# Optimization experiments

Measured on AMD Instinct MI355X. Metric: run time of the kernel, lower is better.

## Reference

```python
import jax, jax.numpy as jnp
import numpy as np

WS = 8
HEADS = 8


def _conv3(x, w, groups=1):
    return jax.lax.conv_general_dilated(
        x, w, (1, 1), 'SAME',
        dimension_numbers=('NCHW', 'OIHW', 'NCHW'),
        feature_group_count=groups)


def _bn(x, g, b, eps=1e-5):
    # training-mode batchnorm (batch statistics), per-channel over (B,H,W)
    m = x.mean(axis=(0, 2, 3), keepdims=True)
    v = x.var(axis=(0, 2, 3), keepdims=True)
    return (x - m) * jax.lax.rsqrt(v + eps) * g[None, :, None, None] + b[None, :, None, None]


def _relu6(x):
    return jnp.clip(x, 0.0, 6.0)


def _forward(x, w_iem, g_iem, b_iem, w_nem, g_nem, b_nem,
             w_iem_dw, w_nem_dw, w_q, w_k, w_v, w_proj, temperature):
    b, C, hp, wp = x.shape
    heads = temperature.shape[1]
    d = C // heads
    ws = WS
    nh, nw = hp // ws, wp // ws  # H,W chosen divisible by ws -> no padding

    iem_out = _relu6(_bn(_conv3(x, w_iem), g_iem, b_iem))
    illumination_map = _conv3(iem_out, w_iem_dw, groups=C)
    nem_out = _relu6(_bn(_conv3(x, w_nem), g_nem, b_nem))
    noise_map = _conv3(nem_out, w_nem_dw, groups=C)

    illum_scalar = illumination_map.mean(axis=1, keepdims=True)  # [b,1,H,W]
    noise_scalar = noise_map.mean(axis=1, keepdims=True)

    # 1x1 convs as channel matmuls
    q = jnp.einsum('oc,bchw->bohw', w_q, illumination_map)
    k = jnp.einsum('oc,bchw->bohw', w_k, noise_map)
    v = jnp.einsum('oc,bchw->bohw', w_v, x)

    def to_windows(t):  # [b,C,H,W] -> [b,heads,nh,nw,ws*ws,d]
        t = t.reshape(b, heads, d, hp, wp).transpose(0, 1, 3, 4, 2)
        t = t.reshape(b, heads, nh, ws, nw, ws, d).transpose(0, 1, 2, 4, 3, 5, 6)
        return t.reshape(b, heads, nh, nw, ws * ws, d)

    def scalar_to_windows(t):  # [b,1,H,W] -> [b,1,nh,nw,ws*ws,1]
        t = t.reshape(b, 1, nh, ws, nw, ws).transpose(0, 1, 2, 4, 3, 5)
        return t.reshape(b, 1, nh, nw, ws * ws, 1)

    qw, kw, vw = to_windows(q), to_windows(k), to_windows(v)
    illum_w = scalar_to_windows(illum_scalar)
    noise_w = scalar_to_windows(noise_scalar)

    qw = qw / jnp.maximum(jnp.linalg.norm(qw, axis=-1, keepdims=True), 1e-12)
    kw = kw / jnp.maximum(jnp.linalg.norm(kw, axis=-1, keepdims=True), 1e-12)
    qw = qw * (1.0 + illum_w)
    kw = kw * jnp.clip(1.0 - noise_w, 0.0, 1.0)

    scale = d ** (-0.5)
    attn = jnp.einsum('bhnmqd,bhnmkd->bhnmqk', qw, kw) * scale
    attn = attn * temperature  # temperature: [1,heads,1,1,1,1]
    attn = jax.nn.softmax(attn, axis=-1)
    outw = jnp.einsum('bhnmqk,bhnmkd->bhnmqd', attn, vw)

    outw = outw.reshape(b, heads, nh, nw, ws, ws, d).transpose(0, 1, 6, 2, 4, 3, 5)
    out = outw.reshape(b, C, hp, wp)
    return jnp.einsum('oc,bchw->bohw', w_proj, out)


def setup_inputs() -> dict:
    key = jax.random.key(0)
    ks = jax.random.split(key, 10)
    C = 256
    B, H, W = 2, 256, 256

    def w(k, shape):
        return jax.random.normal(k, shape, jnp.float32) * 0.05

    return {
        'x': jax.random.normal(ks[0], (B, C, H, W), jnp.float32),
        'w_iem': w(ks[1], (C, C, 3, 3)),
        'g_iem': jnp.ones((C,), jnp.float32),
        'b_iem': jnp.zeros((C,), jnp.float32),
        'w_nem': w(ks[2], (C, C, 3, 3)),
        'g_nem': jnp.ones((C,), jnp.float32),
        'b_nem': jnp.zeros((C,), jnp.float32),
        'w_iem_dw': w(ks[3], (C, 1, 3, 3)),
        'w_nem_dw': w(ks[4], (C, 1, 3, 3)),
        'w_q': w(ks[5], (C, C)),
        'w_k': w(ks[6], (C, C)),
        'w_v': w(ks[7], (C, C)),
        'w_proj': w(ks[8], (C, C)),
        'temperature': jnp.ones((1, HEADS, 1, 1, 1, 1), jnp.float32),
    }


def reference(x, w_iem, g_iem, b_iem, w_nem, g_nem, b_nem,
              w_iem_dw, w_nem_dw, w_q, w_k, w_v, w_proj, temperature):
    return _forward(x, w_iem, g_iem, b_iem, w_nem, g_nem, b_nem,
                    w_iem_dw, w_nem_dw, w_q, w_k, w_v, w_proj, temperature)
```

## Files before the change

### kernel.cpp

```cpp
#include <hip/hip_runtime.h>
#include <math.h>

constexpr int Bn  = 2;
constexpr int C   = 256;
constexpr int H   = 256;
constexpr int W   = 256;
constexpr int HW  = H * W;
constexpr size_t CHW = (size_t)C * HW;

typedef __bf16 bf16x8 __attribute__((ext_vector_type(8)));
typedef float  f32x4  __attribute__((ext_vector_type(4)));

__device__ __forceinline__ unsigned short f2bf(float f) {
    unsigned int u = __float_as_uint(f);
    u += 0x7fffu + ((u >> 16) & 1u);
    return (unsigned short)(u >> 16);
}
__device__ __forceinline__ float bf2f(unsigned short h) {
    return __uint_as_float(((unsigned int)h) << 16);
}
__device__ __forceinline__ float bflo(unsigned int u) { return __uint_as_float(u << 16); }
__device__ __forceinline__ float bfhi(unsigned int u) { return __uint_as_float(u & 0xffff0000u); }

__device__ __forceinline__ bf16x8 u2b(uint4 u) {
    union { uint4 a; bf16x8 b; } c; c.a = u; return c.b;
}

__device__ __forceinline__ void gld_lds16(const void* g, void* lds) {
    __builtin_amdgcn_global_load_lds(
        (const __attribute__((address_space(1))) unsigned int*)g,
        (__attribute__((address_space(3))) unsigned int*)lds, 16, 0, 0);
}

__device__ __forceinline__ int swz2048(int bid) {
    return ((bid & 7) << 8) | (bid >> 3);
}

__global__ __launch_bounds__(256) void packx_k(
    const float* __restrict__ x, unsigned short* __restrict__ xT)
{
    __shared__ float tl[64][65];
    const int id = blockIdx.x;
    const int ct = id & 3;
    const size_t px0 = (size_t)(id >> 2) * 64;
    const int b  = (int)(px0 >> 16);
    const int hw = (int)(px0 & 65535);
    const int c0 = ct * 64;
    const int t  = threadIdx.x;

    {
        const int cl = t >> 2, pseg = t & 3;
        const float* src = x + ((size_t)(b * C + c0 + cl)) * HW + hw + pseg * 16;
#pragma unroll
        for (int i = 0; i < 4; i++) {
            float4 v = *(const float4*)(src + i * 4);
            tl[cl][pseg * 16 + i * 4 + 0] = v.x;
            tl[cl][pseg * 16 + i * 4 + 1] = v.y;
            tl[cl][pseg * 16 + i * 4 + 2] = v.z;
            tl[cl][pseg * 16 + i * 4 + 3] = v.w;
        }
    }
    __syncthreads();
    {
        const int pl = t >> 2, csec = t & 3;
        __attribute__((aligned(16))) unsigned short rv[16];
#pragma unroll
        for (int j = 0; j < 16; j++) rv[j] = f2bf(tl[csec * 16 + j][pl]);
        unsigned short* dst = xT + (px0 + pl) * C + c0 + csec * 16;
        *(uint4*)dst       = *(const uint4*)&rv[0];
        *(uint4*)(dst + 8) = *(const uint4*)&rv[8];
    }
}

__global__ __launch_bounds__(256) void pack_k(
    const float* __restrict__ w, unsigned short* __restrict__ out, int taps)
{
    const int e = blockIdx.x * 256 + threadIdx.x;
    const int kslot = e & 31;
    const int ocl   = (e >> 5) & 127;
    const int icc   = (e >> 12) & 7;
    const int oct   = (e >> 15) & 1;
    const int off   = e >> 16;
    const int oc = oct * 128 + ocl;
    const int q  = kslot >> 3, j = kslot & 7;
    const int ic = icc * 32 + ((q ^ ((ocl >> 2) & 3)) << 3) + j;
    out[e] = f2bf(w[((size_t)oc * C + ic) * taps + off]);
}

__global__ __launch_bounds__(256, 2) void conv2_k(
    const unsigned short* __restrict__ xT,
    const unsigned short* __restrict__ Wp0, const unsigned short* __restrict__ Wp1,
    unsigned short* __restrict__ out0, unsigned short* __restrict__ out1,
    const unsigned short* __restrict__ zbuf)
{
    __shared__ unsigned short As[2][2][128 * 32];
    __shared__ unsigned short Bs[2][128 * 32];

    const int id  = swz2048(blockIdx.x);
    const int oct = id & 1;
    const int ch  = (id >> 1) & 1;
    const int r   = (id >> 2) & 255;
    const int b   = id >> 10;
    const int px0 = ch * 128;

    const int t  = threadIdx.x;
    const int wv = t >> 6;
    const int l  = t & 63;
    const int wm = (wv >> 1) * 64;
    const int wn = (wv & 1) * 64;

    const int qp = (l >> 4) ^ ((l >> 2) & 3);
    int a_off[4], b_off[4];
#pragma unroll
    for (int i = 0; i < 4; i++) {
        a_off[i] = (wm + i * 16 + (l & 15)) * 64 + qp * 16;
        b_off[i] = (wn + i * 16 + (l & 15)) * 64 + qp * 16;
    }
    const int spx_base = wv * 32 + (l >> 2);
    const int skk0 = (((l & 3) ^ (l >> 4)) << 3);

    const int off_lo = (r == 0) ? 3 : 0;
    const int off_hi = (r == 255) ? 6 : 9;

    f32x4 acc[2][4][4];
#pragma unroll
    for (int s = 0; s < 2; s++)
#pragma unroll
        for (int i = 0; i < 4; i++)
#pragma unroll
            for (int j = 0; j < 4; j++) acc[s][i][j] = (f32x4){0.f, 0.f, 0.f, 0.f};

#pragma unroll 1
    for (int off = off_lo; off < off_hi; ++off) {
        const int dy = off / 3, dx = off - dy * 3;
        const int rr = r + dy - 1;
        const size_t rowpix = (size_t)(b * HW) + (size_t)rr * W;
#pragma unroll 1
        for (int ip = 0; ip < 4; ++ip) {
            __syncthreads();
            const size_t wofs = ((size_t)(((off * 2 + oct) * 8 + ip * 2)) * 4096) * 2
                                + wv * 2048 + l * 16;
#pragma unroll
            for (int kc = 0; kc < 2; kc++) {
                char* A0 = (char*)As[0][kc] + wv * 2048;
                char* A1 = (char*)As[1][kc] + wv * 2048;
                const size_t o = wofs + (size_t)kc * 8192;
                gld_lds16((const char*)Wp0 + o, A0);
                gld_lds16((const char*)Wp0 + o + 1024, A0 + 1024);
                gld_lds16((const char*)Wp1 + o, A1);
                gld_lds16((const char*)Wp1 + o + 1024, A1 + 1024);
                const int ic0 = (ip * 2 + kc) * 32;
                char* BsB = (char*)Bs[kc] + wv * 2048;
#pragma unroll
                for (int i = 0; i < 2; i++) {
                    const int px = spx_base + i * 16;
                    const int cx = px0 + px + dx - 1;
                    const void* g = ((unsigned)cx > 255u)
                        ? (const void*)zbuf
                        : (const void*)(xT + ((rowpix + cx) * C + ic0 + skk0));
                    gld_lds16(g, BsB + i * 1024);
                }
            }
            asm volatile("s_waitcnt vmcnt(0)" ::: "memory");
            __syncthreads();
#pragma unroll
            for (int kc = 0; kc < 2; kc++) {
                bf16x8 af0[4], af1[4], bfr[4];
#pragma unroll
                for (int i = 0; i < 4; i++) {
                    af0[i] = *(const bf16x8*)((const char*)As[0][kc] + a_off[i]);
                    af1[i] = *(const bf16x8*)((const char*)As[1][kc] + a_off[i]);
                }
#pragma unroll
                for (int i = 0; i < 4; i++)
                    bfr[i] = *(const bf16x8*)((const char*)Bs[kc] + b_off[i]);
#pragma unroll
                for (int mi = 0; mi < 4; mi++)
#pragma unroll
                    for (int nj = 0; nj < 4; nj++) {
                        acc[0][mi][nj] = __builtin_amdgcn_mfma_f32_16x16x32_bf16(
                            af0[mi], bfr[nj], acc[0][mi][nj], 0, 0, 0);
                        acc[1][mi][nj] = __builtin_amdgcn_mfma_f32_16x16x32_bf16(
                            af1[mi], bfr[nj], acc[1][mi][nj], 0, 0, 0);
                    }
            }
        }
    }

    const int colpx = px0 + wn + (l & 15);
    const int rowoc = oct * 128 + wm + (l >> 4) * 4;
#pragma unroll
    for (int s = 0; s < 2; s++) {
        unsigned short* ob = s ? out1 : out0;
#pragma unroll
        for (int mi = 0; mi < 4; mi++) {
#pragma unroll
            for (int nj = 0; nj < 4; nj++) {
#pragma unroll
                for (int rg = 0; rg < 4; rg++) {
                    const int oc = rowoc + mi * 16 + rg;
                    const int px = colpx + nj * 16;
                    const size_t idx = ((size_t)(b * C + oc)) * HW + (size_t)r * W + px;
                    ob[idx] = f2bf(acc[s][mi][nj][rg]);
                }
            }
        }
    }
}

__global__ __launch_bounds__(256, 2) void gemm2_k(
    const unsigned short* __restrict__ qin, const unsigned short* __restrict__ kin,
    const unsigned short* __restrict__ Wpq, const unsigned short* __restrict__ Wpk,
    unsigned short* __restrict__ outq, unsigned short* __restrict__ outk)
{
    __shared__ unsigned short As[2][2][128 * 32];
    __shared__ unsigned short Bs[2][2][128 * 32];

    const int id  = swz2048(blockIdx.x);
    const int oct = id & 1;
    const int ch  = (id >> 1) & 1;
    const int r   = (id >> 2) & 255;
    const int b   = id >> 10;
    const int px0 = ch * 128;

    const int t  = threadIdx.x;
    const int wv = t >> 6;
    const int l  = t & 63;
    const int wm = (wv >> 1) * 64;
    const int wn = (wv & 1) * 64;

    const int qp = (l >> 4) ^ ((l >> 2) & 3);
    int a_off[4], b_off[4];
#pragma unroll
    for (int i = 0; i < 4; i++) {
        a_off[i] = (wm + i * 16 + (l & 15)) * 64 + qp * 16;
        b_off[i] = (wn + i * 16 + (l & 15)) * 64 + qp * 16;
    }
    const int spx_base = wv * 32 + (l >> 2);
    const int skk0 = (((l & 3) ^ (l >> 4)) << 3);

    const size_t rowpix = (size_t)(b * HW) + (size_t)r * W;

    f32x4 acc[2][4][4];
#pragma unroll
    for (int s = 0; s < 2; s++)
#pragma unroll
        for (int i = 0; i < 4; i++)
#pragma unroll
            for (int j = 0; j < 4; j++) acc[s][i][j] = (f32x4){0.f, 0.f, 0.f, 0.f};

#pragma unroll 1
    for (int ip = 0; ip < 4; ++ip) {
        __syncthreads();
#pragma unroll
        for (int kc = 0; kc < 2; kc++) {
            const int icc = ip * 2 + kc;
            const size_t wofs = ((size_t)(oct * 8 + icc) * 4096) * 2 + wv * 2048 + l * 16;
            char* Aq = (char*)As[0][kc] + wv * 2048;
            char* Ak = (char*)As[1][kc] + wv * 2048;
            gld_lds16((const char*)Wpq + wofs, Aq);
            gld_lds16((const char*)Wpq + wofs + 1024, Aq + 1024);
            gld_lds16((const char*)Wpk + wofs, Ak);
            gld_lds16((const char*)Wpk + wofs + 1024, Ak + 1024);
            const int ic0 = icc * 32;
            char* Bq = (char*)Bs[0][kc] + wv * 2048;
            char* Bk = (char*)Bs[1][kc] + wv * 2048;
#pragma unroll
            for (int i = 0; i < 2; i++) {
                const int cx = px0 + spx_base + i * 16;
                gld_lds16((const void*)(qin + ((rowpix + cx) * C + ic0 + skk0)), Bq + i * 1024);
                gld_lds16((const void*)(kin + ((rowpix + cx) * C + ic0 + skk0)), Bk + i * 1024);
            }
        }
        asm volatile("s_waitcnt vmcnt(0)" ::: "memory");
        __syncthreads();
#pragma unroll
        for (int kc = 0; kc < 2; kc++) {
#pragma unroll
            for (int s = 0; s < 2; s++) {
                bf16x8 af[4], bfr[4];
#pragma unroll
                for (int i = 0; i < 4; i++) {
                    af[i]  = *(const bf16x8*)((const char*)As[s][kc] + a_off[i]);
                    bfr[i] = *(const bf16x8*)((const char*)Bs[s][kc] + b_off[i]);
                }
#pragma unroll
                for (int mi = 0; mi < 4; mi++)
#pragma unroll
                    for (int nj = 0; nj < 4; nj++)
                        acc[s][mi][nj] = __builtin_amdgcn_mfma_f32_16x16x32_bf16(
                            af[mi], bfr[nj], acc[s][mi][nj], 0, 0, 0);
            }
        }
    }

    const int colpx = px0 + wn + (l & 15);
    const int rowoc = oct * 128 + wm + (l >> 4) * 4;
    const size_t pxg = (size_t)(b * HW) + (size_t)r * W;
#pragma unroll
    for (int s = 0; s < 2; s++) {
        unsigned short* ob = s ? outk : outq;
#pragma unroll
        for (int mi = 0; mi < 4; mi++) {
#pragma unroll
            for (int nj = 0; nj < 4; nj++) {
                __attribute__((aligned(8))) unsigned short rv[4];
#pragma unroll
                for (int rg = 0; rg < 4; rg++) rv[rg] = f2bf(acc[s][mi][nj][rg]);
                const int oc = rowoc + mi * 16;
                const int px = colpx + nj * 16;
                *(uint2*)(ob + (pxg + px) * C + oc) = *(const uint2*)rv;
            }
        }
    }
}

template<bool F32OUT, bool NHWC_OUT>
__global__ __launch_bounds__(256, 2) void gemm_k(
    const unsigned short* __restrict__ xT, const unsigned short* __restrict__ Wp,
    unsigned short* __restrict__ outb, float* __restrict__ outf)
{
    __shared__ unsigned short As[2][128 * 32];
    __shared__ unsigned short Bs[2][128 * 32];

    const int id  = swz2048(blockIdx.x);
    const int oct = id & 1;
    const int ch  = (id >> 1) & 1;
    const int r   = (id >> 2) & 255;
    const int b   = id >> 10;
    const int px0 = ch * 128;

    const int t  = threadIdx.x;
    const int wv = t >> 6;
    const int l  = t & 63;
    const int wm = (wv >> 1) * 64;
    const int wn = (wv & 1) * 64;

    const int qp = (l >> 4) ^ ((l >> 2) & 3);
    int a_off[4], b_off[4];
#pragma unroll
    for (int i = 0; i < 4; i++) {
        a_off[i] = (wm + i * 16 + (l & 15)) * 64 + qp * 16;
        b_off[i] = (wn + i * 16 + (l & 15)) * 64 + qp * 16;
    }
    const int spx_base = wv * 32 + (l >> 2);
    const int skk0 = (((l & 3) ^ (l >> 4)) << 3);

    const size_t rowpix = (size_t)(b * HW) + (size_t)r * W;

    f32x4 acc[4][4];
#pragma unroll
    for (int i = 0; i < 4; i++)
#pragma unroll
        for (int j = 0; j < 4; j++) acc[i][j] = (f32x4){0.f, 0.f, 0.f, 0.f};

#pragma unroll 1
    for (int ip = 0; ip < 4; ++ip) {
        __syncthreads();
#pragma unroll
        for (int kc = 0; kc < 2; kc++) {
            const int icc = ip * 2 + kc;
            const char* Ag = (const char*)Wp +
                ((size_t)(oct * 8 + icc) * 4096) * 2 + wv * 2048 + l * 16;
            char* AsB = (char*)As[kc] + wv * 2048;
            gld_lds16(Ag, AsB);
            gld_lds16(Ag + 1024, AsB + 1024);
            const int ic0 = icc * 32;
            char* BsB = (char*)Bs[kc] + wv * 2048;
#pragma unroll
            for (int i = 0; i < 2; i++) {
                const int cx = px0 + spx_base + i * 16;
                gld_lds16((const void*)(xT + ((rowpix + cx) * C + ic0 + skk0)), BsB + i * 1024);
            }
        }
        asm volatile("s_waitcnt vmcnt(0)" ::: "memory");
        __syncthreads();
#pragma unroll
        for (int kc = 0; kc < 2; kc++) {
            bf16x8 af[4], bfr[4];
#pragma unroll
            for (int i = 0; i < 4; i++) {
                af[i]  = *(const bf16x8*)((const char*)As[kc] + a_off[i]);
                bfr[i] = *(const bf16x8*)((const char*)Bs[kc] + b_off[i]);
            }
#pragma unroll
            for (int mi = 0; mi < 4; mi++)
#pragma unroll
                for (int nj = 0; nj < 4; nj++)
                    acc[mi][nj] = __builtin_amdgcn_mfma_f32_16x16x32_bf16(
                        af[mi], bfr[nj], acc[mi][nj], 0, 0, 0);
        }
    }

    const int colpx = px0 + wn + (l & 15);
    const int rowoc = oct * 128 + wm + (l >> 4) * 4;
    if (NHWC_OUT) {
        const size_t pxg = (size_t)(b * HW) + (size_t)r * W;
#pragma unroll
        for (int mi = 0; mi < 4; mi++) {
#pragma unroll
            for (int nj = 0; nj < 4; nj++) {
                __attribute__((aligned(8))) unsigned short rv[4];
#pragma unroll
                for (int rg = 0; rg < 4; rg++) rv[rg] = f2bf(acc[mi][nj][rg]);
                const int oc = rowoc + mi * 16;
                const int px = colpx + nj * 16;
                *(uint2*)(outb + (pxg + px) * C + oc) = *(const uint2*)rv;
            }
        }
    } else {
#pragma unroll
        for (int mi = 0; mi < 4; mi++) {
#pragma unroll
            for (int nj = 0; nj < 4; nj++) {
#pragma unroll
                for (int rg = 0; rg < 4; rg++) {
                    const int oc = rowoc + mi * 16 + rg;
                    const int px = colpx + nj * 16;
                    const size_t idx = ((size_t)(b * C + oc)) * HW + (size_t)r * W + px;
                    if (F32OUT) outf[idx] = acc[mi][nj][rg];
                    else        outb[idx] = f2bf(acc[mi][nj][rg]);
                }
            }
        }
    }
}

__global__ __launch_bounds__(256) void bnstats_k(
    const unsigned short* __restrict__ a, const float* __restrict__ g,
    const float* __restrict__ beta, float* __restrict__ scale, float* __restrict__ shift)
{
    const int c = blockIdx.x;
    const int t = threadIdx.x;
    float s = 0.f, ss = 0.f;
    for (int b = 0; b < Bn; b++) {
        const uint4* p = (const uint4*)(a + ((size_t)(b * C + c)) * HW);
        for (int i = t; i < HW / 8; i += 256) {
            uint4 v = p[i];
            float f0 = bflo(v.x), f1 = bfhi(v.x), f2 = bflo(v.y), f3 = bfhi(v.y);
            float f4 = bflo(v.z), f5 = bfhi(v.z), f6 = bflo(v.w), f7 = bfhi(v.w);
            s  += (f0 + f1) + (f2 + f3) + (f4 + f5) + (f6 + f7);
            ss += f0*f0 + f1*f1 + f2*f2 + f3*f3 + f4*f4 + f5*f5 + f6*f6 + f7*f7;
        }
    }
    __shared__ float rs[256], rss[256];
    rs[t] = s; rss[t] = ss;
    __syncthreads();
    for (int o = 128; o > 0; o >>= 1) {
        if (t < o) { rs[t] += rs[t + o]; rss[t] += rss[t + o]; }
        __syncthreads();
    }
    if (t == 0) {
        const float n    = (float)Bn * HW;
        const float mean = rs[0] / n;
        const float var  = rss[0] / n - mean * mean;
        const float sc   = g[c] * rsqrtf(var + 1e-5f);
        scale[c] = sc;
        shift[c] = beta[c] - mean * sc;
    }
}

__global__ __launch_bounds__(256) void dwconv_k(
    const unsigned short* __restrict__ a, const float* __restrict__ scale,
    const float* __restrict__ shift, const float* __restrict__ wd,
    unsigned short* __restrict__ out, float* __restrict__ smean)
{
    __shared__ float tile[64][3][67];
    __shared__ float wds[64 * 9];
    __shared__ float sscl[64], sshf[64];

    const int id = blockIdx.x;
    const int c0 = (id & 3) * 64;
    const int w0 = ((id >> 2) & 3) * 64;
    const int r  = (id >> 4) & 255;
    const int b  = id >> 12;
    const int t  = threadIdx.x;

    for (int i = t; i < 576; i += 256) wds[i] = wd[c0 * 9 + i];
    if (t < 64) { sscl[t] = scale[c0 + t]; sshf[t] = shift[c0 + t]; }
    __syncthreads();

    for (int i = t; i < 3072; i += 256) {
        const int c   = i / 48;
        const int rem = i - c * 48;
        const int row = rem >> 4, seg = rem & 15;
        const int rr  = r + row - 1;
        float f0 = 0.f, f1 = 0.f, f2 = 0.f, f3 = 0.f;
        if ((unsigned)rr < 256u) {
            const uint2 v = *(const uint2*)(a + ((size_t)(b * C + c0 + c)) * HW
                                              + (size_t)rr * W + w0 + seg * 4);
            const float sc = sscl[c], sh = sshf[c];
            f0 = fminf(fmaxf(fmaf(bflo(v.x), sc, sh), 0.f), 6.f);
            f1 = fminf(fmaxf(fmaf(bfhi(v.x), sc, sh), 0.f), 6.f);
            f2 = fminf(fmaxf(fmaf(bflo(v.y), sc, sh), 0.f), 6.f);
            f3 = fminf(fmaxf(fmaf(bfhi(v.y), sc, sh), 0.f), 6.f);
        }
        float* dst = &tile[c][row][1 + seg * 4];
        dst[0] = f0; dst[1] = f1; dst[2] = f2; dst[3] = f3;
    }
    for (int i = t; i < 384; i += 256) {
        const int c   = i / 6;
        const int rem = i - c * 6;
        const int row = rem >> 1, side = rem & 1;
        const int rr  = r + row - 1;
        const int col = side ? (w0 + 64) : (w0 - 1);
        float v = 0.f;
        if ((unsigned)rr < 256u && (unsigned)col < 256u) {
            float u = bf2f(a[((size_t)(b * C + c0 + c)) * HW + (size_t)rr * W + col]);
            v = fminf(fmaxf(fmaf(u, sscl[c], sshf[c]), 0.f), 6.f);
        }
        tile[c][row][side ? 65 : 0] = v;
    }
    __syncthreads();

    const int px = t >> 2, csub = t & 3;
    __attribute__((aligned(16))) unsigned short res[16];
    float psum = 0.f;
#pragma unroll
    for (int k = 0; k < 16; k++) {
        const int c = csub * 16 + k;
        const float* wp = &wds[c * 9];
        float accv = 0.f;
#pragma unroll
        for (int dy = 0; dy < 3; dy++)
#pragma unroll
            for (int dx = 0; dx < 3; dx++)
                accv = fmaf(tile[c][dy][px + dx], wp[dy * 3 + dx], accv);
        res[k] = f2bf(accv);
        psum += accv;
    }
    unsigned short* o = out + ((size_t)(b * HW) + (size_t)r * W + w0 + px) * C + c0 + csub * 16;
    *(uint4*)o       = *(const uint4*)&res[0];
    *(uint4*)(o + 8) = *(const uint4*)&res[8];

    psum += __shfl_xor(psum, 1);
    psum += __shfl_xor(psum, 2);
    if (csub == 0)
        atomicAdd(&smean[(size_t)(b * HW) + (size_t)r * W + w0 + px], psum * (1.f / C));
}

__global__ __launch_bounds__(64) void attn_k(
    const unsigned short* __restrict__ q, const unsigned short* __restrict__ k,
    const unsigned short* __restrict__ v, const float* __restrict__ si,
    const float* __restrict__ sn, const float* __restrict__ temp,
    unsigned short* __restrict__ out)
{
    __shared__ unsigned short Pl[64][72];
    __shared__ unsigned short Vt[32][72];

    const int id   = blockIdx.x;
    const int wx   = id & 31;
    const int wy   = (id >> 5) & 31;
    const int head = (id >> 10) & 7;
    const int b    = id >> 13;
    const int l    = threadIdx.x;
    const int pl15 = l & 15;
    const int g    = l >> 4;
    const int ch0  = head * 32;
    const int base = wy * 8 * W + wx * 8;
    const size_t bb = (size_t)b * HW;

    uint4 qv[4], kv[4];
    float qss[4], kss[4];
#pragma unroll
    for (int i = 0; i < 4; i++) {
        const int p = i * 16 + pl15;
        const size_t a = (bb + base + (p >> 3) * W + (p & 7)) * C + ch0 + g * 8;
        qv[i] = *(const uint4*)(q + a);
        kv[i] = *(const uint4*)(k + a);
        float s0 = 0.f, s1 = 0.f;
        {
            uint4 u = qv[i];
            float f;
            f = bflo(u.x); s0 = fmaf(f, f, s0);  f = bfhi(u.x); s0 = fmaf(f, f, s0);
            f = bflo(u.y); s0 = fmaf(f, f, s0);  f = bfhi(u.y); s0 = fmaf(f, f, s0);
            f = bflo(u.z); s0 = fmaf(f, f, s0);  f = bfhi(u.z); s0 = fmaf(f, f, s0);
            f = bflo(u.w); s0 = fmaf(f, f, s0);  f = bfhi(u.w); s0 = fmaf(f, f, s0);
        }
        {
            uint4 u = kv[i];
            float f;
            f = bflo(u.x); s1 = fmaf(f, f, s1);  f = bfhi(u.x); s1 = fmaf(f, f, s1);
            f = bflo(u.y); s1 = fmaf(f, f, s1);  f = bfhi(u.y); s1 = fmaf(f, f, s1);
            f = bflo(u.z); s1 = fmaf(f, f, s1);  f = bfhi(u.z); s1 = fmaf(f, f, s1);
            f = bflo(u.w); s1 = fmaf(f, f, s1);  f = bfhi(u.w); s1 = fmaf(f, f, s1);
        }
        s0 += __shfl_xor(s0, 16); s0 += __shfl_xor(s0, 32);
        s1 += __shfl_xor(s1, 16); s1 += __shfl_xor(s1, 32);
        qss[i] = s0; kss[i] = s1;
    }

    {
        const size_t a = (bb + base + (l >> 3) * W + (l & 7)) * C + ch0;
        const uint4* vp = (const uint4*)(v + a);
#pragma unroll
        for (int i = 0; i < 4; i++) {
            uint4 vv = vp[i];
            Vt[i * 8 + 0][l] = (unsigned short)(vv.x);
            Vt[i * 8 + 1][l] = (unsigned short)(vv.x >> 16);
            Vt[i * 8 + 2][l] = (unsigned short)(vv.y);
            Vt[i * 8 + 3][l] = (unsigned short)(vv.y >> 16);
            Vt[i * 8 + 4][l] = (unsigned short)(vv.z);
            Vt[i * 8 + 5][l] = (unsigned short)(vv.z >> 16);
            Vt[i * 8 + 6][l] = (unsigned short)(vv.w);
            Vt[i * 8 + 7][l] = (unsigned short)(vv.w >> 16);
        }
    }

    const float tsc = temp[head] * 0.17677669529663689f;
    float qmul[4], kscl[4];
#pragma unroll
    for (int i = 0; i < 4; i++) {
        const int p = i * 16 + pl15;
        const size_t pg = bb + base + (p >> 3) * W + (p & 7);
        const float il = si[pg];
        const float nz = sn[pg];
        qmul[i] = (1.f + il) * tsc / fmaxf(sqrtf(qss[i]), 1e-12f);
        kscl[i] = fminf(fmaxf(1.f - nz, 0.f), 1.f) / fmaxf(sqrtf(kss[i]), 1e-12f);
    }

    f32x4 acc[4][4];
#pragma unroll
    for (int qi = 0; qi < 4; qi++)
#pragma unroll
        for (int kj = 0; kj < 4; kj++)
            acc[qi][kj] = __builtin_amdgcn_mfma_f32_16x16x32_bf16(
                u2b(qv[qi]), u2b(kv[kj]), (f32x4){0.f, 0.f, 0.f, 0.f}, 0, 0, 0);

    float inv[4][4];
#pragma unroll
    for (int qi = 0; qi < 4; qi++) {
#pragma unroll
        for (int rg = 0; rg < 4; rg++) {
            const float qm = __shfl(qmul[qi], (g << 2) + rg);
            float s[4];
#pragma unroll
            for (int kj = 0; kj < 4; kj++) s[kj] = acc[qi][kj][rg] * kscl[kj] * qm;
            float mx = fmaxf(fmaxf(s[0], s[1]), fmaxf(s[2], s[3]));
            mx = fmaxf(mx, __shfl_xor(mx, 1));
            mx = fmaxf(mx, __shfl_xor(mx, 2));
            mx = fmaxf(mx, __shfl_xor(mx, 4));
            mx = fmaxf(mx, __shfl_xor(mx, 8));
            float sum = 0.f;
#pragma unroll
            for (int kj = 0; kj < 4; kj++) {
                const float e = __expf(s[kj] - mx);
                acc[qi][kj][rg] = e;
                sum += e;
            }
            sum += __shfl_xor(sum, 1);
            sum += __shfl_xor(sum, 2);
            sum += __shfl_xor(sum, 4);
            sum += __shfl_xor(sum, 8);
            inv[qi][rg] = 1.f / sum;
            const int qrow = qi * 16 + (g << 2) + rg;
#pragma unroll
            for (int kj = 0; kj < 4; kj++)
                Pl[qrow][pl15 + 16 * kj] = f2bf(acc[qi][kj][rg]);
        }
    }

    f32x4 oacc[4][2];
#pragma unroll
    for (int qi = 0; qi < 4; qi++)
#pragma unroll
        for (int dj = 0; dj < 2; dj++) oacc[qi][dj] = (f32x4){0.f, 0.f, 0.f, 0.f};

#pragma unroll
    for (int kc = 0; kc < 2; kc++) {
        const bf16x8 vb0 = *(const bf16x8*)&Vt[pl15][kc * 32 + g * 8];
        const bf16x8 vb1 = *(const bf16x8*)&Vt[pl15 + 16][kc * 32 + g * 8];
#pragma unroll
        for (int qi = 0; qi < 4; qi++) {
            const bf16x8 pa = *(const bf16x8*)&Pl[qi * 16 + pl15][kc * 32 + g * 8];
            oacc[qi][0] = __builtin_amdgcn_mfma_f32_16x16x32_bf16(pa, vb0, oacc[qi][0], 0, 0, 0);
            oacc[qi][1] = __builtin_amdgcn_mfma_f32_16x16x32_bf16(pa, vb1, oacc[qi][1], 0, 0, 0);
        }
    }

#pragma unroll
    for (int qi = 0; qi < 4; qi++) {
#pragma unroll
        for (int rg = 0; rg < 4; rg++) {
            const int qrow = qi * 16 + (g << 2) + rg;
            const size_t oaddr = (bb + base + (qrow >> 3) * W + (qrow & 7)) * C + ch0;
            const float sc = inv[qi][rg];
            out[oaddr + pl15]      = f2bf(oacc[qi][0][rg] * sc);
            out[oaddr + 16 + pl15] = f2bf(oacc[qi][1][rg] * sc);
        }
    }
}

extern "C" void kernel_launch(void* const* d_in, const int* in_sizes, int n_in,
                              void* d_out, int out_size, void* d_ws, size_t ws_size,
                              hipStream_t stream)
{
    const float* x        = (const float*)d_in[0];
    const float* w_iem    = (const float*)d_in[1];
    const float* g_iem    = (const float*)d_in[2];
    const float* b_iem    = (const float*)d_in[3];
    const float* w_nem    = (const float*)d_in[4];
    const float* g_nem    = (const float*)d_in[5];
    const float* b_nem    = (const float*)d_in[6];
    const float* w_iem_dw = (const float*)d_in[7];
    const float* w_nem_dw = (const float*)d_in[8];
    const float* w_q      = (const float*)d_in[9];
    const float* w_k      = (const float*)d_in[10];
    const float* w_v      = (const float*)d_in[11];
    const float* w_proj   = (const float*)d_in[12];
    const float* temp     = (const float*)d_in[13];

    char* p = (char*)d_ws;
    unsigned short* zbuf = (unsigned short*)p;      p += 256;
    float* scl = (float*)p;                         p += 256 * 4;
    float* shf = (float*)p;                         p += 256 * 4;
    float* sI  = (float*)p;                         p += (size_t)Bn * HW * 4;
    float* sN  = (float*)p;                         p += (size_t)Bn * HW * 4;
    unsigned short* Wp_iem = (unsigned short*)p;    p += 589824 * 2;
    unsigned short* Wp_nem = (unsigned short*)p;    p += 589824 * 2;
    unsigned short* Wpq = (unsigned short*)p;       p += 65536 * 2;
    unsigned short* Wpk = (unsigned short*)p;       p += 65536 * 2;
    unsigned short* Wpv = (unsigned short*)p;       p += 65536 * 2;
    unsigned short* Wpp = (unsigned short*)p;       p += 65536 * 2;
    unsigned short* xT   = (unsigned short*)p;      p += Bn * CHW * 2;
    unsigned short* bufA = (unsigned short*)p;      p += Bn * CHW * 2;
    unsigned short* Ibf  = (unsigned short*)p;      p += Bn * CHW * 2;
    unsigned short* Nbf  = (unsigned short*)p;      p += Bn * CHW * 2;
    unsigned short* Obf  = (unsigned short*)p;      p += Bn * CHW * 2;

    hipMemsetAsync(zbuf, 0, 256, stream);
    hipMemsetAsync(sI, 0, (size_t)Bn * HW * 4, stream);
    hipMemsetAsync(sN, 0, (size_t)Bn * HW * 4, stream);

    packx_k<<<8192, 256, 0, stream>>>(x, xT);
    pack_k<<<2304, 256, 0, stream>>>(w_iem, Wp_iem, 9);
    pack_k<<<2304, 256, 0, stream>>>(w_nem, Wp_nem, 9);
    pack_k<<<256, 256, 0, stream>>>(w_q, Wpq, 1);
    pack_k<<<256, 256, 0, stream>>>(w_k, Wpk, 1);
    pack_k<<<256, 256, 0, stream>>>(w_v, Wpv, 1);
    pack_k<<<256, 256, 0, stream>>>(w_proj, Wpp, 1);

    conv2_k<<<2048, 256, 0, stream>>>(xT, Wp_iem, Wp_nem, bufA, Obf, zbuf);

    bnstats_k<<<256, 256, 0, stream>>>(bufA, g_iem, b_iem, scl, shf);
    dwconv_k<<<8192, 256, 0, stream>>>(bufA, scl, shf, w_iem_dw, Ibf, sI);
    bnstats_k<<<256, 256, 0, stream>>>(Obf, g_nem, b_nem, scl, shf);
    dwconv_k<<<8192, 256, 0, stream>>>(Obf, scl, shf, w_nem_dw, Nbf, sN);

    gemm2_k<<<2048, 256, 0, stream>>>(Ibf, Nbf, Wpq, Wpk, bufA, Obf);
    gemm_k<false, true><<<2048, 256, 0, stream>>>(xT, Wpv, Nbf, nullptr);

    attn_k<<<16384, 64, 0, stream>>>(bufA, Obf, Nbf, sI, sN, temp, Ibf);

    gemm_k<true, false><<<2048, 256, 0, stream>>>(Ibf, Wpp, nullptr, (float*)d_out);
}
```

Baseline: 1.163 ms.

## Fuse BN statistics into conv epilogue, merge weight packing, raise MFMA priority

The conv epilogue now reduces per-channel sum and sum-of-squares with wave shuffles and atomically adds them into a stats buffer. A single small finalize kernel then computes the scale and shift for both branches, replacing two bnstats passes that each re-read a full bf16 activation tensor. The four 1x1 weight-pack launches are merged into one kernel, the two memsets are combined, and s_setprio is added around the MFMA blocks in attention. Statistics now come from fp32 accumulators rather than the bf16-rounded values, and the atomics make the summation order nondeterministic.

```diff
diff --git a/kernel.cpp b/kernel.cpp
--- a/kernel.cpp
+++ b/kernel.cpp
@@ -87,11 +87,32 @@
     out[e] = f2bf(w[((size_t)oc * C + ic) * taps + off]);
 }
 
+__global__ __launch_bounds__(256) void pack4_k(
+    const float* __restrict__ wq, const float* __restrict__ wk,
+    const float* __restrict__ wv, const float* __restrict__ wp,
+    unsigned short* __restrict__ oq, unsigned short* __restrict__ ok,
+    unsigned short* __restrict__ ov, unsigned short* __restrict__ op)
+{
+    const int bid  = blockIdx.x;
+    const int wsel = bid >> 8;
+    const int e    = (bid & 255) * 256 + threadIdx.x;
+    const float* w = (wsel == 0) ? wq : (wsel == 1) ? wk : (wsel == 2) ? wv : wp;
+    unsigned short* out = (wsel == 0) ? oq : (wsel == 1) ? ok : (wsel == 2) ? ov : op;
+    const int kslot = e & 31;
+    const int ocl   = (e >> 5) & 127;
+    const int icc   = (e >> 12) & 7;
+    const int oct   = (e >> 15) & 1;
+    const int oc = oct * 128 + ocl;
+    const int q  = kslot >> 3, j = kslot & 7;
+    const int ic = icc * 32 + ((q ^ ((ocl >> 2) & 3)) << 3) + j;
+    out[e] = f2bf(w[(size_t)oc * C + ic]);
+}
+
 __global__ __launch_bounds__(256, 2) void conv2_k(
     const unsigned short* __restrict__ xT,
     const unsigned short* __restrict__ Wp0, const unsigned short* __restrict__ Wp1,
     unsigned short* __restrict__ out0, unsigned short* __restrict__ out1,
-    const unsigned short* __restrict__ zbuf)
+    const unsigned short* __restrict__ zbuf, float* __restrict__ stats)
 {
     __shared__ unsigned short As[2][2][128 * 32];
     __shared__ unsigned short Bs[2][128 * 32];
@@ -192,19 +213,57 @@
 #pragma unroll
     for (int s = 0; s < 2; s++) {
         unsigned short* ob = s ? out1 : out0;
+        float* sums = stats + s * 512;
 #pragma unroll
         for (int mi = 0; mi < 4; mi++) {
 #pragma unroll
-            for (int nj = 0; nj < 4; nj++) {
-#pragma unroll
-                for (int rg = 0; rg < 4; rg++) {
-                    const int oc = rowoc + mi * 16 + rg;
+            for (int rg = 0; rg < 4; rg++) {
+                const int oc = rowoc + mi * 16 + rg;
+                float ps = 0.f, pq = 0.f;
+#pragma unroll
+                for (int nj = 0; nj < 4; nj++) {
+                    const float v = acc[s][mi][nj][rg];
+                    ps += v;
+                    pq = fmaf(v, v, pq);
                     const int px = colpx + nj * 16;
                     const size_t idx = ((size_t)(b * C + oc)) * HW + (size_t)r * W + px;
-                    ob[idx] = f2bf(acc[s][mi][nj][rg]);
+                    ob[idx] = f2bf(v);
                 }
-            }
-        }
+                ps += __shfl_xor(ps, 1);  pq += __shfl_xor(pq, 1);
+                ps += __shfl_xor(ps, 2);  pq += __shfl_xor(pq, 2);
+                ps += __shfl_xor(ps, 4);  pq += __shfl_xor(pq, 4);
+                ps += __shfl_xor(ps, 8);  pq += __shfl_xor(pq, 8);
+                if ((l & 15) == 0) {
+                    atomicAdd(&sums[oc], ps);
+                    atomicAdd(&sums[256 + oc], pq);
+                }
+            }
+        }
+    }
+}
+
+__global__ __launch_bounds__(256) void bnfin_k(
+    const float* __restrict__ stats,
+    const float* __restrict__ g0, const float* __restrict__ b0,
+    const float* __restrict__ g1, const float* __restrict__ b1,
+    float* __restrict__ scl0, float* __restrict__ shf0,
+    float* __restrict__ scl1, float* __restrict__ shf1)
+{
+    const int c = threadIdx.x;
+    const float n = (float)Bn * HW;
+    {
+        const float mean = stats[c] / n;
+        const float var  = stats[256 + c] / n - mean * mean;
+        const float sc   = g0[c] * rsqrtf(var + 1e-5f);
+        scl0[c] = sc;
+        shf0[c] = b0[c] - mean * sc;
+    }
+    {
+        const float mean = stats[512 + c] / n;
+        const float var  = stats[768 + c] / n - mean * mean;
+        const float sc   = g1[c] * rsqrtf(var + 1e-5f);
+        scl1[c] = sc;
+        shf1[c] = b1[c] - mean * sc;
     }
 }
 
@@ -423,40 +482,6 @@
                 }
             }
         }
-    }
-}
-
-__global__ __launch_bounds__(256) void bnstats_k(
-    const unsigned short* __restrict__ a, const float* __restrict__ g,
-    const float* __restrict__ beta, float* __restrict__ scale, float* __restrict__ shift)
-{
-    const int c = blockIdx.x;
-    const int t = threadIdx.x;
-    float s = 0.f, ss = 0.f;
-    for (int b = 0; b < Bn; b++) {
-        const uint4* p = (const uint4*)(a + ((size_t)(b * C + c)) * HW);
-        for (int i = t; i < HW / 8; i += 256) {
-            uint4 v = p[i];
-            float f0 = bflo(v.x), f1 = bfhi(v.x), f2 = bflo(v.y), f3 = bfhi(v.y);
-            float f4 = bflo(v.z), f5 = bfhi(v.z), f6 = bflo(v.w), f7 = bfhi(v.w);
-            s  += (f0 + f1) + (f2 + f3) + (f4 + f5) + (f6 + f7);
-            ss += f0*f0 + f1*f1 + f2*f2 + f3*f3 + f4*f4 + f5*f5 + f6*f6 + f7*f7;
-        }
-    }
-    __shared__ float rs[256], rss[256];
-    rs[t] = s; rss[t] = ss;
-    __syncthreads();
-    for (int o = 128; o > 0; o >>= 1) {
-        if (t < o) { rs[t] += rs[t + o]; rss[t] += rss[t + o]; }
-        __syncthreads();
-    }
-    if (t == 0) {
-        const float n    = (float)Bn * HW;
-        const float mean = rs[0] / n;
-        const float var  = rss[0] / n - mean * mean;
-        const float sc   = g[c] * rsqrtf(var + 1e-5f);
-        scale[c] = sc;
-        shift[c] = beta[c] - mean * sc;
     }
 }
 
@@ -620,12 +645,14 @@
     }
 
     f32x4 acc[4][4];
+    __builtin_amdgcn_s_setprio(1);
 #pragma unroll
     for (int qi = 0; qi < 4; qi++)
 #pragma unroll
         for (int kj = 0; kj < 4; kj++)
             acc[qi][kj] = __builtin_amdgcn_mfma_f32_16x16x32_bf16(
                 u2b(qv[qi]), u2b(kv[kj]), (f32x4){0.f, 0.f, 0.f, 0.f}, 0, 0, 0);
+    __builtin_amdgcn_s_setprio(0);
 
     float inv[4][4];
 #pragma unroll
@@ -670,12 +697,14 @@
     for (int kc = 0; kc < 2; kc++) {
         const bf16x8 vb0 = *(const bf16x8*)&Vt[pl15][kc * 32 + g * 8];
         const bf16x8 vb1 = *(const bf16x8*)&Vt[pl15 + 16][kc * 32 + g * 8];
+        __builtin_amdgcn_s_setprio(1);
 #pragma unroll
         for (int qi = 0; qi < 4; qi++) {
             const bf16x8 pa = *(const bf16x8*)&Pl[qi * 16 + pl15][kc * 32 + g * 8];
             oacc[qi][0] = __builtin_amdgcn_mfma_f32_16x16x32_bf16(pa, vb0, oacc[qi][0], 0, 0, 0);
             oacc[qi][1] = __builtin_amdgcn_mfma_f32_16x16x32_bf16(pa, vb1, oacc[qi][1], 0, 0, 0);
         }
+        __builtin_amdgcn_s_setprio(0);
     }
 
 #pragma unroll
@@ -712,8 +741,11 @@
 
     char* p = (char*)d_ws;
     unsigned short* zbuf = (unsigned short*)p;      p += 256;
-    float* scl = (float*)p;                         p += 256 * 4;
-    float* shf = (float*)p;                         p += 256 * 4;
+    float* scl0 = (float*)p;                        p += 256 * 4;
+    float* shf0 = (float*)p;                        p += 256 * 4;
+    float* scl1 = (float*)p;                        p += 256 * 4;
+    float* shf1 = (float*)p;                        p += 256 * 4;
+    float* stats = (float*)p;                       p += 1024 * 4;
     float* sI  = (float*)p;                         p += (size_t)Bn * HW * 4;
     float* sN  = (float*)p;                         p += (size_t)Bn * HW * 4;
     unsigned short* Wp_iem = (unsigned short*)p;    p += 589824 * 2;
@@ -729,23 +761,20 @@
     unsigned short* Obf  = (unsigned short*)p;      p += Bn * CHW * 2;
 
     hipMemsetAsync(zbuf, 0, 256, stream);
-    hipMemsetAsync(sI, 0, (size_t)Bn * HW * 4, stream);
-    hipMemsetAsync(sN, 0, (size_t)Bn * HW * 4, stream);
+    hipMemsetAsync(stats, 0, 1024 * 4, stream);
+    hipMemsetAsync(sI, 0, (size_t)Bn * HW * 4 * 2, stream);
 
     packx_k<<<8192, 256, 0, stream>>>(x, xT);
     pack_k<<<2304, 256, 0, stream>>>(w_iem, Wp_iem, 9);
     pack_k<<<2304, 256, 0, stream>>>(w_nem, Wp_nem, 9);
-    pack_k<<<256, 256, 0, stream>>>(w_q, Wpq, 1);
-    pack_k<<<256, 256, 0, stream>>>(w_k, Wpk, 1);
-    pack_k<<<256, 256, 0, stream>>>(w_v, Wpv, 1);
-    pack_k<<<256, 256, 0, stream>>>(w_proj, Wpp, 1);
-
-    conv2_k<<<2048, 256, 0, stream>>>(xT, Wp_iem, Wp_nem, bufA, Obf, zbuf);
-
-    bnstats_k<<<256, 256, 0, stream>>>(bufA, g_iem, b_iem, scl, shf);
-    dwconv_k<<<8192, 256, 0, stream>>>(bufA, scl, shf, w_iem_dw, Ibf, sI);
-    bnstats_k<<<256, 256, 0, stream>>>(Obf, g_nem, b_nem, scl, shf);
-    dwconv_k<<<8192, 256, 0, stream>>>(Obf, scl, shf, w_nem_dw, Nbf, sN);
+    pack4_k<<<1024, 256, 0, stream>>>(w_q, w_k, w_v, w_proj, Wpq, Wpk, Wpv, Wpp);
+
+    conv2_k<<<2048, 256, 0, stream>>>(xT, Wp_iem, Wp_nem, bufA, Obf, zbuf, stats);
+    bnfin_k<<<1, 256, 0, stream>>>(stats, g_iem, b_iem, g_nem, b_nem,
+                                   scl0, shf0, scl1, shf1);
+
+    dwconv_k<<<8192, 256, 0, stream>>>(bufA, scl0, shf0, w_iem_dw, Ibf, sI);
+    dwconv_k<<<8192, 256, 0, stream>>>(Obf, scl1, shf1, w_nem_dw, Nbf, sN);
 
     gemm2_k<<<2048, 256, 0, stream>>>(Ibf, Nbf, Wpq, Wpk, bufA, Obf);
     gemm_k<false, true><<<2048, 256, 0, stream>>>(xT, Wpv, Nbf, nullptr);
```

After: 1.236 ms. 1.06x slower.
